# Optimization experiments

Measured on AMD Instinct MI355X. Metric: run time of the kernel, lower is better.

The kernel has to match this reference:

```python
import jax, jax.numpy as jnp
import numpy as np

LAMBDA = 1.0


def _sq_dists(x, y):
    # x: (B,N,3), y: (B,M,3) -> (B,N,M) squared euclidean distances
    x2 = jnp.sum(x * x, axis=-1)  # (B,N)
    y2 = jnp.sum(y * y, axis=-1)  # (B,M)
    xy = jnp.einsum('bnd,bmd->bnm', x, y)  # (B,N,M)
    return x2[:, :, None] + y2[:, None, :] - 2.0 * xy


def setup_inputs() -> dict:
    key = jax.random.key(0)
    k1, k2, k3 = jax.random.split(key, 3)
    B, N = 4, 8192
    pc_pred = jax.random.normal(k1, (B, N, 3), dtype=jnp.float32)
    pc_target = jax.random.normal(k2, (B, N, 3), dtype=jnp.float32)
    fbpp = jax.random.uniform(k3, (1,), dtype=jnp.float32)
    return {"pc_pred": pc_pred, "pc_target": pc_target, "fbpp": fbpp}


def reference(pc_pred, pc_target, fbpp):
    # Chamfer distance (pytorch3d semantics): squared L2 1-NN both directions,
    # mean over points, mean over batch, summed over the two directions.
    d2 = _sq_dists(pc_pred, pc_target)  # (B,N,M)
    cham_x = jnp.mean(jnp.min(d2, axis=2), axis=1)  # (B,) pred -> target
    cham_y = jnp.mean(jnp.min(d2, axis=1), axis=1)  # (B,) target -> pred
    dist = jnp.mean(cham_x) + jnp.mean(cham_y)
    rate = jnp.mean(fbpp)
    loss = dist + LAMBDA * rate
    return (loss, dist, rate)
```

## Files before the change

### kernel.cpp

```cpp
#include <hip/hip_runtime.h>
#include <math.h>

typedef _Float16 f16x8 __attribute__((ext_vector_type(8)));
typedef __fp16   fp16v2 __attribute__((ext_vector_type(2)));
typedef float    f32x16 __attribute__((ext_vector_type(16)));

#define THREADS 256
#define YCHUNK  4096
#define XPB     128

static __device__ inline unsigned pk2(float a, float b) {
    fp16v2 h = __builtin_amdgcn_cvt_pkrtz(a, b);
    return __builtin_bit_cast(unsigned, h);
}

__global__ __launch_bounds__(THREADS, 2) void chamfer_kernel(
    const float* __restrict__ pred, const float* __restrict__ targ,
    float* __restrict__ partials, int N)
{
    const int dir = blockIdx.z;
    const float* xsrc = dir == 0 ? pred : targ;
    const float* ysrc = dir == 0 ? targ : pred;
    const int b = blockIdx.y;

    __shared__ uint2 sy[YCHUNK];
    __shared__ float swave[4];

    const int tid  = threadIdx.x;
    const int lane = tid & 63;
    const int wave = tid >> 6;
    const int col  = lane & 31;

    const size_t xi = (size_t)(b * N + blockIdx.x * XPB + wave * 32 + col) * 3;
    const float x0 = xsrc[xi], x1 = xsrc[xi + 1], x2 = xsrc[xi + 2];

    const bool act = lane < 32;
    f16x8 bf;
    bf[0] = act ? (_Float16)(-2.0f * x0) : (_Float16)0.0f;
    bf[1] = act ? (_Float16)(-2.0f * x1) : (_Float16)0.0f;
    bf[2] = act ? (_Float16)(-2.0f * x2) : (_Float16)0.0f;
    bf[3] = act ? (_Float16)1.0f : (_Float16)0.0f;
    bf[4] = bf[5] = bf[6] = bf[7] = (_Float16)0.0f;

    f32x16 zacc;
    f32x16 vmin;
#pragma unroll
    for (int r = 0; r < 16; ++r) { zacc[r] = 0.0f; vmin[r] = INFINITY; }

    const float* ybase = ysrc + (size_t)b * N * 3;
    const int nchunks = N / YCHUNK;

    for (int c = 0; c < nchunks; ++c) {
        __syncthreads();
#pragma unroll
        for (int j = 0; j < YCHUNK / THREADS; ++j) {
            const int    yj = j * THREADS + tid;
            const float* yp = ybase + (size_t)(c * YCHUNK + yj) * 3;
            float y0 = yp[0], y1 = yp[1], y2v = yp[2];
            float nn = fmaf(y0, y0, fmaf(y1, y1, y2v * y2v));
            sy[yj] = make_uint2(pk2(y0, y1), pk2(y2v, nn));
        }
        __syncthreads();

#define LOADJ(j) uint2 lo##j = sy[(i + j) * 32 + col]
#define MFJ(j)                                                            \
        f32x16 ac##j = __builtin_amdgcn_mfma_f32_32x32x16_f16(            \
            __builtin_bit_cast(f16x8,                                     \
                make_uint4(lo##j.x, lo##j.y, 0u, 0u)), bf, zacc, 0, 0, 0)
        for (int i = 0; i < YCHUNK / 32; i += 8) {
            LOADJ(0); LOADJ(1); LOADJ(2); LOADJ(3);
            LOADJ(4); LOADJ(5); LOADJ(6); LOADJ(7);
            MFJ(0); MFJ(1); MFJ(2); MFJ(3);
            MFJ(4); MFJ(5); MFJ(6); MFJ(7);
#pragma unroll
            for (int r = 0; r < 16; ++r) {
                vmin[r] = fminf(fminf(vmin[r], ac0[r]), ac1[r]);
                vmin[r] = fminf(fminf(vmin[r], ac2[r]), ac3[r]);
                vmin[r] = fminf(fminf(vmin[r], ac4[r]), ac5[r]);
                vmin[r] = fminf(fminf(vmin[r], ac6[r]), ac7[r]);
            }
        }
#undef LOADJ
#undef MFJ
    }

    float v = vmin[0];
#pragma unroll
    for (int r = 1; r < 16; ++r) v = fminf(v, vmin[r]);
    v = fminf(v, __shfl_xor(v, 32));
    float d = v + fmaf(x0, x0, fmaf(x1, x1, x2 * x2));

#pragma unroll
    for (int off = 16; off > 0; off >>= 1) d += __shfl_xor(d, off);
    if (lane == 0) swave[wave] = d;
    __syncthreads();
    if (tid == 0) {
        float s = swave[0] + swave[1] + swave[2] + swave[3];
        int bid = blockIdx.x + gridDim.x * (blockIdx.y + gridDim.y * blockIdx.z);
        partials[bid] = s;
    }
}

__global__ __launch_bounds__(512) void finalize(
    const float* __restrict__ partials, const float* __restrict__ fbpp,
    float* __restrict__ out, int nPerDir, int totalPts)
{
    __shared__ float sw[8];
    const int tid = threadIdx.x;
    float v = (tid < 2 * nPerDir) ? partials[tid] : 0.0f;
#pragma unroll
    for (int off = 32; off > 0; off >>= 1) v += __shfl_xor(v, off);
    if ((tid & 63) == 0) sw[tid >> 6] = v;
    __syncthreads();
    if (tid == 0) {
        float s0 = sw[0] + sw[1] + sw[2] + sw[3];
        float s1 = sw[4] + sw[5] + sw[6] + sw[7];
        float inv = 1.0f / (float)totalPts;
        float dist = s0 * inv + s1 * inv;
        float rate = fbpp[0];
        out[0] = dist + rate;
        out[1] = dist;
        out[2] = rate;
    }
}

extern "C" void kernel_launch(void* const* d_in, const int* in_sizes, int n_in,
                              void* d_out, int out_size, void* d_ws, size_t ws_size,
                              hipStream_t stream) {
    const float* pred = (const float*)d_in[0];
    const float* targ = (const float*)d_in[1];
    const float* fbpp = (const float*)d_in[2];
    float* out = (float*)d_out;

    const int B = 4;
    const int N = in_sizes[0] / (B * 3);
    float* partials = (float*)d_ws;

    dim3 grid(N / XPB, B, 2);
    chamfer_kernel<<<grid, THREADS, 0, stream>>>(pred, targ, partials, N);

    const int nPerDir = (N / XPB) * B;
    finalize<<<1, 512, 0, stream>>>(partials, fbpp, out, nPerDir, B * N);
}
```

Before: 24.89 us.

## Fuse final reduction via atomic last-block pattern and vectorize y-chunk loads

Replaces the separate finalize kernel with a global atomic accumulator plus a last-block-done counter, so the final loss is written inside the main kernel. A tiny init kernel zeroes the accumulator, so there are still two launches. The y-chunk staging now reads float4 vectors, with each thread packing four points instead of one strided scalar triple. Float atomic summation makes the result order-nondeterministic, and the shared-memory write pattern changes.

```diff
diff --git a/kernel.cpp b/kernel.cpp
--- a/kernel.cpp
+++ b/kernel.cpp
@@ -14,9 +14,15 @@
     return __builtin_bit_cast(unsigned, h);
 }
 
+__global__ void init_accum(float* __restrict__ ws) {
+    ws[0] = 0.0f;
+    ((int*)ws)[1] = 0;
+}
+
 __global__ __launch_bounds__(THREADS, 2) void chamfer_kernel(
     const float* __restrict__ pred, const float* __restrict__ targ,
-    float* __restrict__ partials, int N)
+    float* __restrict__ accum, const float* __restrict__ fbpp,
+    float* __restrict__ out, int N, int nBlocks)
 {
     const int dir = blockIdx.z;
     const float* xsrc = dir == 0 ? pred : targ;
@@ -52,13 +58,22 @@
 
     for (int c = 0; c < nchunks; ++c) {
         __syncthreads();
+        const float4* yf4 = (const float4*)(ybase + (size_t)c * YCHUNK * 3);
 #pragma unroll
-        for (int j = 0; j < YCHUNK / THREADS; ++j) {
-            const int    yj = j * THREADS + tid;
-            const float* yp = ybase + (size_t)(c * YCHUNK + yj) * 3;
-            float y0 = yp[0], y1 = yp[1], y2v = yp[2];
-            float nn = fmaf(y0, y0, fmaf(y1, y1, y2v * y2v));
-            sy[yj] = make_uint2(pk2(y0, y1), pk2(y2v, nn));
+        for (int k = 0; k < 4; ++k) {
+            const int fbase = k * THREADS * 3 + tid * 3;
+            float4 f0 = yf4[fbase + 0];
+            float4 f1 = yf4[fbase + 1];
+            float4 f2 = yf4[fbase + 2];
+            const int yj = (k * THREADS + tid) * 4;
+            float n0 = fmaf(f0.x, f0.x, fmaf(f0.y, f0.y, f0.z * f0.z));
+            float n1 = fmaf(f0.w, f0.w, fmaf(f1.x, f1.x, f1.y * f1.y));
+            float n2 = fmaf(f1.z, f1.z, fmaf(f1.w, f1.w, f2.x * f2.x));
+            float n3 = fmaf(f2.y, f2.y, fmaf(f2.z, f2.z, f2.w * f2.w));
+            sy[yj + 0] = make_uint2(pk2(f0.x, f0.y), pk2(f0.z, n0));
+            sy[yj + 1] = make_uint2(pk2(f0.w, f1.x), pk2(f1.y, n1));
+            sy[yj + 2] = make_uint2(pk2(f1.z, f1.w), pk2(f2.x, n2));
+            sy[yj + 3] = make_uint2(pk2(f2.y, f2.z), pk2(f2.w, n3));
         }
         __syncthreads();
 
@@ -94,33 +109,21 @@
     for (int off = 16; off > 0; off >>= 1) d += __shfl_xor(d, off);
     if (lane == 0) swave[wave] = d;
     __syncthreads();
+
     if (tid == 0) {
         float s = swave[0] + swave[1] + swave[2] + swave[3];
-        int bid = blockIdx.x + gridDim.x * (blockIdx.y + gridDim.y * blockIdx.z);
-        partials[bid] = s;
-    }
-}
-
-__global__ __launch_bounds__(512) void finalize(
-    const float* __restrict__ partials, const float* __restrict__ fbpp,
-    float* __restrict__ out, int nPerDir, int totalPts)
-{
-    __shared__ float sw[8];
-    const int tid = threadIdx.x;
-    float v = (tid < 2 * nPerDir) ? partials[tid] : 0.0f;
-#pragma unroll
-    for (int off = 32; off > 0; off >>= 1) v += __shfl_xor(v, off);
-    if ((tid & 63) == 0) sw[tid >> 6] = v;
-    __syncthreads();
-    if (tid == 0) {
-        float s0 = sw[0] + sw[1] + sw[2] + sw[3];
-        float s1 = sw[4] + sw[5] + sw[6] + sw[7];
-        float inv = 1.0f / (float)totalPts;
-        float dist = s0 * inv + s1 * inv;
-        float rate = fbpp[0];
-        out[0] = dist + rate;
-        out[1] = dist;
-        out[2] = rate;
+        atomicAdd(&accum[0], s);
+        __threadfence();
+        int old = atomicAdd((int*)accum + 1, 1);
+        if (old == nBlocks - 1) {
+            __threadfence();
+            float total = atomicAdd(&accum[0], 0.0f);
+            float dist  = total / (float)(4 * N);
+            float rate  = fbpp[0];
+            out[0] = dist + rate;
+            out[1] = dist;
+            out[2] = rate;
+        }
     }
 }
 
@@ -134,11 +137,12 @@
 
     const int B = 4;
     const int N = in_sizes[0] / (B * 3);
-    float* partials = (float*)d_ws;
+    float* accum = (float*)d_ws;
+
+    init_accum<<<1, 1, 0, stream>>>(accum);
 
     dim3 grid(N / XPB, B, 2);
-    chamfer_kernel<<<grid, THREADS, 0, stream>>>(pred, targ, partials, N);
-
-    const int nPerDir = (N / XPB) * B;
-    finalize<<<1, 512, 0, stream>>>(partials, fbpp, out, nPerDir, B * N);
+    const int nBlocks = grid.x * grid.y * grid.z;
+    chamfer_kernel<<<grid, THREADS, 0, stream>>>(pred, targ, accum, fbpp,
+                                                 out, N, nBlocks);
 }
```

Result: slower. 35.47 us (+42.5%).

## Double-buffer Y chunks in LDS and prefetch second chunk with float4 loads

Applied to the files above, without the earlier changes.

Splits the Y staging into two LDS buffers and issues global loads for the second chunk before computing on the first, so load latency overlaps the MFMA loop. Y loads become vectorized float4 reads that pack four points per thread. This hardcodes N=8192 (two chunks, fixed offsets) and doubles LDS use to 64KB per block, which may reduce occupancy. It also keeps 48 extra registers live through the first compute loop.

```diff
diff --git a/kernel.cpp b/kernel.cpp
--- a/kernel.cpp
+++ b/kernel.cpp
@@ -14,6 +14,18 @@
     return __builtin_bit_cast(unsigned, h);
 }
 
+static __device__ inline void packwrite(uint2* dst, float4 f0, float4 f1,
+                                        float4 f2) {
+    float n0 = fmaf(f0.x, f0.x, fmaf(f0.y, f0.y, f0.z * f0.z));
+    float n1 = fmaf(f0.w, f0.w, fmaf(f1.x, f1.x, f1.y * f1.y));
+    float n2 = fmaf(f1.z, f1.z, fmaf(f1.w, f1.w, f2.x * f2.x));
+    float n3 = fmaf(f2.y, f2.y, fmaf(f2.z, f2.z, f2.w * f2.w));
+    dst[0] = make_uint2(pk2(f0.x, f0.y), pk2(f0.z, n0));
+    dst[1] = make_uint2(pk2(f0.w, f1.x), pk2(f1.y, n1));
+    dst[2] = make_uint2(pk2(f1.z, f1.w), pk2(f2.x, n2));
+    dst[3] = make_uint2(pk2(f2.y, f2.z), pk2(f2.w, n3));
+}
+
 __global__ __launch_bounds__(THREADS, 2) void chamfer_kernel(
     const float* __restrict__ pred, const float* __restrict__ targ,
     float* __restrict__ partials, int N)
@@ -23,7 +35,8 @@
     const float* ysrc = dir == 0 ? targ : pred;
     const int b = blockIdx.y;
 
-    __shared__ uint2 sy[YCHUNK];
+    __shared__ uint2 sy0[YCHUNK];
+    __shared__ uint2 sy1[YCHUNK];
     __shared__ float swave[4];
 
     const int tid  = threadIdx.x;
@@ -47,42 +60,56 @@
 #pragma unroll
     for (int r = 0; r < 16; ++r) { zacc[r] = 0.0f; vmin[r] = INFINITY; }
 
-    const float* ybase = ysrc + (size_t)b * N * 3;
-    const int nchunks = N / YCHUNK;
+    const float4* yf4 = (const float4*)(ysrc + (size_t)b * N * 3);
 
-    for (int c = 0; c < nchunks; ++c) {
-        __syncthreads();
 #pragma unroll
-        for (int j = 0; j < YCHUNK / THREADS; ++j) {
-            const int    yj = j * THREADS + tid;
-            const float* yp = ybase + (size_t)(c * YCHUNK + yj) * 3;
-            float y0 = yp[0], y1 = yp[1], y2v = yp[2];
-            float nn = fmaf(y0, y0, fmaf(y1, y1, y2v * y2v));
-            sy[yj] = make_uint2(pk2(y0, y1), pk2(y2v, nn));
-        }
-        __syncthreads();
+    for (int k = 0; k < 4; ++k) {
+        const int fb = k * THREADS * 3 + tid * 3;
+        packwrite(&sy0[(k * THREADS + tid) * 4], yf4[fb], yf4[fb + 1],
+                  yf4[fb + 2]);
+    }
 
-#define LOADJ(j) uint2 lo##j = sy[(i + j) * 32 + col]
-#define MFJ(j)                                                            \
-        f32x16 ac##j = __builtin_amdgcn_mfma_f32_32x32x16_f16(            \
-            __builtin_bit_cast(f16x8,                                     \
-                make_uint4(lo##j.x, lo##j.y, 0u, 0u)), bf, zacc, 0, 0, 0)
-        for (int i = 0; i < YCHUNK / 32; i += 8) {
-            LOADJ(0); LOADJ(1); LOADJ(2); LOADJ(3);
-            LOADJ(4); LOADJ(5); LOADJ(6); LOADJ(7);
-            MFJ(0); MFJ(1); MFJ(2); MFJ(3);
-            MFJ(4); MFJ(5); MFJ(6); MFJ(7);
-#pragma unroll
-            for (int r = 0; r < 16; ++r) {
-                vmin[r] = fminf(fminf(vmin[r], ac0[r]), ac1[r]);
-                vmin[r] = fminf(fminf(vmin[r], ac2[r]), ac3[r]);
-                vmin[r] = fminf(fminf(vmin[r], ac4[r]), ac5[r]);
-                vmin[r] = fminf(fminf(vmin[r], ac6[r]), ac7[r]);
-            }
-        }
+#define GDECL(k)                                                           \
+    float4 g##k##a = yf4[3072 + k * THREADS * 3 + tid * 3 + 0];            \
+    float4 g##k##b = yf4[3072 + k * THREADS * 3 + tid * 3 + 1];            \
+    float4 g##k##c = yf4[3072 + k * THREADS * 3 + tid * 3 + 2]
+    GDECL(0); GDECL(1); GDECL(2); GDECL(3);
+#undef GDECL
+
+    __syncthreads();
+
+#define LOADJ(j, SY) uint2 lo##j = SY[(i + j) * 32 + col]
+#define MFJ(j)                                                             \
+    f32x16 ac##j = __builtin_amdgcn_mfma_f32_32x32x16_f16(                 \
+        __builtin_bit_cast(f16x8,                                          \
+            make_uint4(lo##j.x, lo##j.y, 0u, 0u)), bf, zacc, 0, 0, 0)
+#define COMPUTE(SY)                                                        \
+    for (int i = 0; i < YCHUNK / 32; i += 8) {                             \
+        LOADJ(0, SY); LOADJ(1, SY); LOADJ(2, SY); LOADJ(3, SY);            \
+        LOADJ(4, SY); LOADJ(5, SY); LOADJ(6, SY); LOADJ(7, SY);            \
+        MFJ(0); MFJ(1); MFJ(2); MFJ(3);                                    \
+        MFJ(4); MFJ(5); MFJ(6); MFJ(7);                                    \
+        _Pragma("unroll")                                                  \
+        for (int r = 0; r < 16; ++r) {                                     \
+            vmin[r] = fminf(fminf(vmin[r], ac0[r]), ac1[r]);               \
+            vmin[r] = fminf(fminf(vmin[r], ac2[r]), ac3[r]);               \
+            vmin[r] = fminf(fminf(vmin[r], ac4[r]), ac5[r]);               \
+            vmin[r] = fminf(fminf(vmin[r], ac6[r]), ac7[r]);               \
+        }                                                                  \
+    }
+
+    COMPUTE(sy0)
+
+    packwrite(&sy1[(0 * THREADS + tid) * 4], g0a, g0b, g0c);
+    packwrite(&sy1[(1 * THREADS + tid) * 4], g1a, g1b, g1c);
+    packwrite(&sy1[(2 * THREADS + tid) * 4], g2a, g2b, g2c);
+    packwrite(&sy1[(3 * THREADS + tid) * 4], g3a, g3b, g3c);
+    __syncthreads();
+
+    COMPUTE(sy1)
+#undef COMPUTE
 #undef LOADJ
 #undef MFJ
-    }
 
     float v = vmin[0];
 #pragma unroll
@@ -103,20 +130,20 @@
 
 __global__ __launch_bounds__(512) void finalize(
     const float* __restrict__ partials, const float* __restrict__ fbpp,
-    float* __restrict__ out, int nPerDir, int totalPts)
+    float* __restrict__ out, int nPartials, int totalPts)
 {
     __shared__ float sw[8];
     const int tid = threadIdx.x;
-    float v = (tid < 2 * nPerDir) ? partials[tid] : 0.0f;
+    float v = (tid < nPartials) ? partials[tid] : 0.0f;
 #pragma unroll
     for (int off = 32; off > 0; off >>= 1) v += __shfl_xor(v, off);
     if ((tid & 63) == 0) sw[tid >> 6] = v;
     __syncthreads();
     if (tid == 0) {
-        float s0 = sw[0] + sw[1] + sw[2] + sw[3];
-        float s1 = sw[4] + sw[5] + sw[6] + sw[7];
-        float inv = 1.0f / (float)totalPts;
-        float dist = s0 * inv + s1 * inv;
+        float t = 0.0f;
+#pragma unroll
+        for (int w = 0; w < 8; ++w) t += sw[w];
+        float dist = t / (float)totalPts;
         float rate = fbpp[0];
         out[0] = dist + rate;
         out[1] = dist;
@@ -139,6 +166,6 @@
     dim3 grid(N / XPB, B, 2);
     chamfer_kernel<<<grid, THREADS, 0, stream>>>(pred, targ, partials, N);
 
-    const int nPerDir = (N / XPB) * B;
-    finalize<<<1, 512, 0, stream>>>(partials, fbpp, out, nPerDir, B * N);
+    const int nPartials = (N / XPB) * B * 2;
+    finalize<<<1, 512, 0, stream>>>(partials, fbpp, out, nPartials, B * N);
 }
```

Result: no change. 24.52 us (-1.5%).
